# Optimization experiments

Measured on AMD Instinct MI355X. Metric: run time of the kernel, lower is better.

Reference implementation:

```python
import jax, jax.numpy as jnp
from jax import lax
import numpy as np

HIDDEN = 16
INPUT = 1
OUTPUT = 1
BATCH = 8192
SEQ = 512


def setup_inputs() -> dict:
    key = jax.random.key(0)
    ks = jax.random.split(key, 12)
    s = 1.0 / np.sqrt(HIDDEN)  # PyTorch nn.RNN init scale
    u = lambda k, shape: jax.random.uniform(k, shape, jnp.float32, -s, s)
    return {
        "x": jax.random.normal(ks[0], (BATCH, SEQ, INPUT), jnp.float32),
        "W_ih0": u(ks[1], (HIDDEN, INPUT)),
        "W_hh0": u(ks[2], (HIDDEN, HIDDEN)),
        "b_ih0": u(ks[3], (HIDDEN,)),
        "b_hh0": u(ks[4], (HIDDEN,)),
        "W_ih1": u(ks[5], (HIDDEN, HIDDEN)),
        "W_hh1": u(ks[6], (HIDDEN, HIDDEN)),
        "b_ih1": u(ks[7], (HIDDEN,)),
        "b_hh1": u(ks[8], (HIDDEN,)),
        "W_fc": u(ks[9], (OUTPUT, HIDDEN)),
        "b_fc": u(ks[10], (OUTPUT,)),
    }


def reference(x, W_ih0, W_hh0, b_ih0, b_hh0, W_ih1, W_hh1, b_ih1, b_hh1, W_fc, b_fc):
    # x: [B, S, input]; 2-layer tanh RNN (batch_first), zero initial state,
    # then fc applied to the last timestep of the top layer.
    B = x.shape[0]
    h_init = (jnp.zeros((B, HIDDEN), x.dtype), jnp.zeros((B, HIDDEN), x.dtype))

    def step(carry, xt):  # xt: [B, input]
        h0, h1 = carry
        h0 = jnp.tanh(xt @ W_ih0.T + b_ih0 + h0 @ W_hh0.T + b_hh0)
        h1 = jnp.tanh(h0 @ W_ih1.T + b_ih1 + h1 @ W_hh1.T + b_hh1)
        return (h0, h1), None

    xs = jnp.swapaxes(x, 0, 1)  # [S, B, input] for scan over time
    (h0, h1), _ = lax.scan(step, h_init, xs)
    return h1 @ W_fc.T + b_fc  # [B, output]
```

## Files before the change

### kernel.cpp

```cpp
#include <hip/hip_runtime.h>
#include <hip/hip_fp16.h>


typedef __fp16 f16x4 __attribute__((ext_vector_type(4)));
typedef __fp16 f16x2 __attribute__((ext_vector_type(2)));
typedef float  f32x4 __attribute__((ext_vector_type(4)));

__device__ __forceinline__ float tanh_fast(float v) {
    float e = __builtin_amdgcn_exp2f(v * 2.8853900817779268f);
    float r = __builtin_amdgcn_rcpf(e + 1.0f);
    return fmaf(-2.0f, r, 1.0f);
}

__global__ __launch_bounds__(64, 1) void rnn2_mfma(
    const float* __restrict__ x,
    const float* __restrict__ Wih0, const float* __restrict__ Whh0,
    const float* __restrict__ bih0, const float* __restrict__ bhh0,
    const float* __restrict__ Wih1, const float* __restrict__ Whh1,
    const float* __restrict__ bih1, const float* __restrict__ bhh1,
    const float* __restrict__ Wfc,  const float* __restrict__ bfc,
    float* __restrict__ out)
{
    const int lane = threadIdx.x & 63;
    const int q    = lane >> 4;
    const int col  = lane & 15;
    const int m4   = q * 4;
    const int b0   = blockIdx.x * 16;

    f16x4 Ahh0, Aih1, Ahh1;
#pragma unroll
    for (int i = 0; i < 4; ++i) {
        Ahh0[i] = (__fp16)Whh0[col * 16 + m4 + i];
        Aih1[i] = (__fp16)Wih1[col * 16 + m4 + i];
        Ahh1[i] = (__fp16)Whh1[col * 16 + m4 + i];
    }
    float wih0q[4], b0q[4], wfcq[4];
    f32x4 cb1;
#pragma unroll
    for (int r = 0; r < 4; ++r) {
        wih0q[r] = Wih0[m4 + r];
        b0q[r]   = bih0[m4 + r] + bhh0[m4 + r];
        cb1[r]   = bih1[m4 + r] + bhh1[m4 + r];
        wfcq[r]  = Wfc[m4 + r];
    }
    const float* __restrict__ xrow = x + (size_t)(b0 + col) * 512;

    f16x4 Bh0 = {0, 0, 0, 0}, Bh1 = {0, 0, 0, 0};
    const f32x4 zero4 = {0.f, 0.f, 0.f, 0.f};
    float u0 = 0.f, u1 = 0.f, u2 = 0.f, u3 = 0.f;

    float xc[16], xn[16];
#pragma unroll
    for (int i = 0; i < 16; ++i) xc[i] = xrow[i];

    for (int t0 = 0; t0 < 512; t0 += 16) {
        const int tn = (t0 + 16) & 511;
#pragma unroll
        for (int i = 0; i < 16; ++i) xn[i] = xrow[tn + i];

#pragma unroll
        for (int j = 0; j < 16; ++j) {
            const float xt = xc[j];
            f32x4 c0;
            c0[0] = fmaf(wih0q[0], xt, b0q[0]);
            c0[1] = fmaf(wih0q[1], xt, b0q[1]);
            c0[2] = fmaf(wih0q[2], xt, b0q[2]);
            c0[3] = fmaf(wih0q[3], xt, b0q[3]);

            f32x4 a = __builtin_amdgcn_mfma_f32_16x16x16f16(Ahh0, Bh0, c0, 0, 0, 0);
            const float s0 = tanh_fast(a[0]);
            const float s1 = tanh_fast(a[1]);
            const float s2 = tanh_fast(a[2]);
            const float s3 = tanh_fast(a[3]);
            f16x2 p0 = __builtin_amdgcn_cvt_pkrtz(s0, s1);
            f16x2 p1 = __builtin_amdgcn_cvt_pkrtz(s2, s3);
            Bh0 = __builtin_shufflevector(p0, p1, 0, 1, 2, 3);

            f32x4 d = __builtin_amdgcn_mfma_f32_16x16x16f16(Aih1, Bh0, cb1, 0, 0, 0);
            f32x4 e = __builtin_amdgcn_mfma_f32_16x16x16f16(Ahh1, Bh1, zero4, 0, 0, 0);
            u0 = tanh_fast(d[0] + e[0]);
            u1 = tanh_fast(d[1] + e[1]);
            u2 = tanh_fast(d[2] + e[2]);
            u3 = tanh_fast(d[3] + e[3]);
            f16x2 r0 = __builtin_amdgcn_cvt_pkrtz(u0, u1);
            f16x2 r1 = __builtin_amdgcn_cvt_pkrtz(u2, u3);
            Bh1 = __builtin_shufflevector(r0, r1, 0, 1, 2, 3);
        }
#pragma unroll
        for (int i = 0; i < 16; ++i) xc[i] = xn[i];
    }

    float v = u0 * wfcq[0] + u1 * wfcq[1] + u2 * wfcq[2] + u3 * wfcq[3];
    v += __shfl_xor(v, 16, 64);
    v += __shfl_xor(v, 32, 64);
    if (lane < 16) out[b0 + lane] = v + bfc[0];
}

extern "C" void kernel_launch(void* const* d_in, const int* in_sizes, int n_in,
                              void* d_out, int out_size, void* d_ws, size_t ws_size,
                              hipStream_t stream) {
    const float* x    = (const float*)d_in[0];
    const float* Wih0 = (const float*)d_in[1];
    const float* Whh0 = (const float*)d_in[2];
    const float* bih0 = (const float*)d_in[3];
    const float* bhh0 = (const float*)d_in[4];
    const float* Wih1 = (const float*)d_in[5];
    const float* Whh1 = (const float*)d_in[6];
    const float* bih1 = (const float*)d_in[7];
    const float* bhh1 = (const float*)d_in[8];
    const float* Wfc  = (const float*)d_in[9];
    const float* bfc  = (const float*)d_in[10];
    float* out = (float*)d_out;

    rnn2_mfma<<<dim3(512), dim3(64), 0, stream>>>(
        x, Wih0, Whh0, bih0, bhh0, Wih1, Whh1, bih1, bhh1, Wfc, bfc, out);
}
```

Baseline: 172.1 us.

## Pipeline RNN layers across two waves via shared-memory ring buffer

```diff
diff --git a/kernel.cpp b/kernel.cpp
--- a/kernel.cpp
+++ b/kernel.cpp
@@ -12,7 +12,7 @@
     return fmaf(-2.0f, r, 1.0f);
 }
 
-__global__ __launch_bounds__(64, 1) void rnn2_mfma(
+__global__ __launch_bounds__(128, 1) void rnn2_pipek(
     const float* __restrict__ x,
     const float* __restrict__ Wih0, const float* __restrict__ Whh0,
     const float* __restrict__ bih0, const float* __restrict__ bhh0,
@@ -21,11 +21,15 @@
     const float* __restrict__ Wfc,  const float* __restrict__ bfc,
     float* __restrict__ out)
 {
-    const int lane = threadIdx.x & 63;
+    const int tid  = threadIdx.x;
+    const int wid  = tid >> 6;
+    const int lane = tid & 63;
     const int q    = lane >> 4;
     const int col  = lane & 15;
     const int m4   = q * 4;
     const int b0   = blockIdx.x * 16;
+
+    __shared__ unsigned long long h0slot[32][64];
 
     f16x4 Ahh0, Aih1, Ahh1;
 #pragma unroll
@@ -44,56 +48,69 @@
         wfcq[r]  = Wfc[m4 + r];
     }
     const float* __restrict__ xrow = x + (size_t)(b0 + col) * 512;
+    const f32x4 zero4 = {0.f, 0.f, 0.f, 0.f};
 
-    f16x4 Bh0 = {0, 0, 0, 0}, Bh1 = {0, 0, 0, 0};
-    const f32x4 zero4 = {0.f, 0.f, 0.f, 0.f};
+    f16x4 Bh0 = {0, 0, 0, 0};
+    float xc[16], xn[16];
+    f16x4 h0cur, Bh1 = {0, 0, 0, 0};
     float u0 = 0.f, u1 = 0.f, u2 = 0.f, u3 = 0.f;
 
-    float xc[16], xn[16];
+    if (wid == 0) {
 #pragma unroll
-    for (int i = 0; i < 16; ++i) xc[i] = xrow[i];
-
-    for (int t0 = 0; t0 < 512; t0 += 16) {
-        const int tn = (t0 + 16) & 511;
-#pragma unroll
-        for (int i = 0; i < 16; ++i) xn[i] = xrow[tn + i];
-
-#pragma unroll
-        for (int j = 0; j < 16; ++j) {
-            const float xt = xc[j];
-            f32x4 c0;
-            c0[0] = fmaf(wih0q[0], xt, b0q[0]);
-            c0[1] = fmaf(wih0q[1], xt, b0q[1]);
-            c0[2] = fmaf(wih0q[2], xt, b0q[2]);
-            c0[3] = fmaf(wih0q[3], xt, b0q[3]);
-
-            f32x4 a = __builtin_amdgcn_mfma_f32_16x16x16f16(Ahh0, Bh0, c0, 0, 0, 0);
-            const float s0 = tanh_fast(a[0]);
-            const float s1 = tanh_fast(a[1]);
-            const float s2 = tanh_fast(a[2]);
-            const float s3 = tanh_fast(a[3]);
-            f16x2 p0 = __builtin_amdgcn_cvt_pkrtz(s0, s1);
-            f16x2 p1 = __builtin_amdgcn_cvt_pkrtz(s2, s3);
-            Bh0 = __builtin_shufflevector(p0, p1, 0, 1, 2, 3);
-
-            f32x4 d = __builtin_amdgcn_mfma_f32_16x16x16f16(Aih1, Bh0, cb1, 0, 0, 0);
-            f32x4 e = __builtin_amdgcn_mfma_f32_16x16x16f16(Ahh1, Bh1, zero4, 0, 0, 0);
-            u0 = tanh_fast(d[0] + e[0]);
-            u1 = tanh_fast(d[1] + e[1]);
-            u2 = tanh_fast(d[2] + e[2]);
-            u3 = tanh_fast(d[3] + e[3]);
-            f16x2 r0 = __builtin_amdgcn_cvt_pkrtz(u0, u1);
-            f16x2 r1 = __builtin_amdgcn_cvt_pkrtz(u2, u3);
-            Bh1 = __builtin_shufflevector(r0, r1, 0, 1, 2, 3);
-        }
-#pragma unroll
-        for (int i = 0; i < 16; ++i) xc[i] = xn[i];
+        for (int i = 0; i < 16; ++i) xc[i] = xrow[i];
     }
 
-    float v = u0 * wfcq[0] + u1 * wfcq[1] + u2 * wfcq[2] + u3 * wfcq[3];
-    v += __shfl_xor(v, 16, 64);
-    v += __shfl_xor(v, 32, 64);
-    if (lane < 16) out[b0 + lane] = v + bfc[0];
+    for (int i = 0; i <= 32; ++i) {
+        if (wid == 0 && i < 32) {
+#pragma unroll
+            for (int k2 = 0; k2 < 16; ++k2)
+                xn[k2] = xrow[((i + 1) * 16 + k2) & 511];
+#pragma unroll
+            for (int j = 0; j < 16; ++j) {
+                const int p = i * 16 + j;
+                const float xt = xc[j];
+                f32x4 c0;
+                c0[0] = fmaf(wih0q[0], xt, b0q[0]);
+                c0[1] = fmaf(wih0q[1], xt, b0q[1]);
+                c0[2] = fmaf(wih0q[2], xt, b0q[2]);
+                c0[3] = fmaf(wih0q[3], xt, b0q[3]);
+                f32x4 a = __builtin_amdgcn_mfma_f32_16x16x16f16(Ahh0, Bh0, c0, 0, 0, 0);
+                f16x2 p0 = __builtin_amdgcn_cvt_pkrtz(tanh_fast(a[0]), tanh_fast(a[1]));
+                f16x2 p1 = __builtin_amdgcn_cvt_pkrtz(tanh_fast(a[2]), tanh_fast(a[3]));
+                Bh0 = __builtin_shufflevector(p0, p1, 0, 1, 2, 3);
+                h0slot[p & 31][lane] = __builtin_bit_cast(unsigned long long, Bh0);
+            }
+#pragma unroll
+            for (int k2 = 0; k2 < 16; ++k2) xc[k2] = xn[k2];
+        }
+        if (wid == 1 && i >= 1) {
+            const int c = i - 1;
+            h0cur = __builtin_bit_cast(f16x4, h0slot[(c * 16) & 31][lane]);
+            unsigned long long h0n_ = 0;
+#pragma unroll
+            for (int j = 0; j < 16; ++j) {
+                if (j < 15) h0n_ = h0slot[(c * 16 + j + 1) & 31][lane];
+                f32x4 d = __builtin_amdgcn_mfma_f32_16x16x16f16(Aih1, h0cur, cb1, 0, 0, 0);
+                f32x4 e = __builtin_amdgcn_mfma_f32_16x16x16f16(Ahh1, Bh1, zero4, 0, 0, 0);
+                u0 = tanh_fast(d[0] + e[0]);
+                u1 = tanh_fast(d[1] + e[1]);
+                u2 = tanh_fast(d[2] + e[2]);
+                u3 = tanh_fast(d[3] + e[3]);
+                f16x2 r0 = __builtin_amdgcn_cvt_pkrtz(u0, u1);
+                f16x2 r1 = __builtin_amdgcn_cvt_pkrtz(u2, u3);
+                Bh1 = __builtin_shufflevector(r0, r1, 0, 1, 2, 3);
+                if (j < 15) h0cur = __builtin_bit_cast(f16x4, h0n_);
+            }
+        }
+        __syncthreads();
+    }
+
+    if (wid == 1) {
+        float v = u0 * wfcq[0] + u1 * wfcq[1] + u2 * wfcq[2] + u3 * wfcq[3];
+        v += __shfl_xor(v, 16, 64);
+        v += __shfl_xor(v, 32, 64);
+        if (lane < 16) out[b0 + lane] = v + bfc[0];
+    }
 }
 
 extern "C" void kernel_launch(void* const* d_in, const int* in_sizes, int n_in,
@@ -112,6 +129,6 @@
     const float* bfc  = (const float*)d_in[10];
     float* out = (float*)d_out;
 
-    rnn2_mfma<<<dim3(512), dim3(64), 0, stream>>>(
+    rnn2_pipek<<<dim3(512), dim3(128), 0, stream>>>(
         x, Wih0, Whh0, bih0, bhh0, Wih1, Whh1, bih1, bhh1, Wfc, bfc, out);
 }
```

After: 167.6 us. -2.6%, faster.
